# Optimization experiments

Measured on AMD Instinct MI355X. Metric: run time of the kernel, lower is better.

Reference implementation:

```python
import jax, jax.numpy as jnp
import numpy as np
from jax import lax

D_MODEL = 60
D_INNER = 120   # expand=2
D_STATE = 16
D_CONV = 4
DT_RANK = 4     # ceil(60/16)
DEPTH = 2
BATCH = 2
H_IMG = 128
W_IMG = 128
L_SEQ = H_IMG * W_IMG


def setup_inputs() -> dict:
    key = jax.random.key(0)
    ks = jax.random.split(key, 12)
    s = 0.02
    x = jax.random.normal(ks[0], (BATCH, L_SEQ, D_MODEL), jnp.float32)
    ln_w = jnp.ones((DEPTH, D_MODEL), jnp.float32)
    ln_b = jnp.zeros((DEPTH, D_MODEL), jnp.float32)
    in_proj_w = jax.random.normal(ks[1], (DEPTH, 2 * D_INNER, D_MODEL), jnp.float32) * s
    conv_w = jax.random.normal(ks[2], (DEPTH, D_INNER, D_CONV), jnp.float32) * s
    conv_b = jnp.zeros((DEPTH, D_INNER), jnp.float32)
    x_proj_w = jax.random.normal(ks[3], (DEPTH, DT_RANK + 2 * D_STATE, D_INNER), jnp.float32) * s
    dt_proj_w = jax.random.normal(ks[4], (DEPTH, D_INNER, DT_RANK), jnp.float32) * s
    dt_proj_b = jnp.full((DEPTH, D_INNER), -4.0, jnp.float32)  # softplus^-1 of small dt
    A_log = jnp.broadcast_to(
        jnp.log(jnp.arange(1, D_STATE + 1, dtype=jnp.float32))[None, None, :],
        (DEPTH, D_INNER, D_STATE)).copy()
    D_skip = jnp.ones((DEPTH, D_INNER), jnp.float32)
    out_proj_w = jax.random.normal(ks[5], (DEPTH, D_MODEL, D_INNER), jnp.float32) * s
    conv2d_w = jax.random.normal(ks[6], (D_MODEL, D_MODEL, 3, 3), jnp.float32) * s
    conv2d_b = jnp.zeros((D_MODEL,), jnp.float32)
    return {"x": x, "ln_w": ln_w, "ln_b": ln_b, "in_proj_w": in_proj_w,
            "conv_w": conv_w, "conv_b": conv_b, "x_proj_w": x_proj_w,
            "dt_proj_w": dt_proj_w, "dt_proj_b": dt_proj_b, "A_log": A_log,
            "D": D_skip, "out_proj_w": out_proj_w,
            "conv2d_w": conv2d_w, "conv2d_b": conv2d_b,
            "H": H_IMG, "W": W_IMG}


def _layernorm(x, w, b, eps=1e-5):
    mu = jnp.mean(x, axis=-1, keepdims=True)
    var = jnp.mean(jnp.square(x - mu), axis=-1, keepdims=True)
    return (x - mu) * lax.rsqrt(var + eps) * w + b


def _selective_scan(dA, dBx, C):
    # dA, dBx: [B, L, D_INNER, D_STATE]; C: [B, L, D_STATE]
    def step(h, inp):
        dA_t, dBx_t, c_t = inp
        h = dA_t * h + dBx_t                       # [B, D_INNER, D_STATE]
        y = jnp.einsum('bdn,bn->bd', h, c_t)
        return h, y
    h0 = jnp.zeros(dA.shape[:1] + dA.shape[2:], dA.dtype)
    _, ys = lax.scan(step, h0,
                     (dA.transpose(1, 0, 2, 3), dBx.transpose(1, 0, 2, 3),
                      C.transpose(1, 0, 2)))
    return ys.transpose(1, 0, 2)                    # [B, L, D_INNER]


def _mamba(x, in_w, cw, cb, xp_w, dtw, dtb, A_log, D_skip, out_w):
    # x: [B, L, D_MODEL]
    xz = jnp.einsum('bld,ed->ble', x, in_w)         # [B, L, 2*D_INNER]
    xin, z = jnp.split(xz, 2, axis=-1)
    # causal depthwise conv1d over L
    xc = xin.transpose(0, 2, 1)                     # [B, D_INNER, L]
    xc = jnp.pad(xc, ((0, 0), (0, 0), (D_CONV - 1, 0)))
    xc = lax.conv_general_dilated(xc, cw[:, None, :], (1,), 'VALID',
                                  dimension_numbers=('NCH', 'OIH', 'NCH'),
                                  feature_group_count=D_INNER)
    xc = jax.nn.silu(xc + cb[None, :, None]).transpose(0, 2, 1)  # [B, L, D_INNER]
    xdb = jnp.einsum('bld,ed->ble', xc, xp_w)       # [B, L, DT_RANK + 2*D_STATE]
    dt = xdb[..., :DT_RANK]
    Bm = xdb[..., DT_RANK:DT_RANK + D_STATE]
    Cm = xdb[..., DT_RANK + D_STATE:]
    delta = jax.nn.softplus(jnp.einsum('blr,dr->bld', dt, dtw) + dtb)  # [B, L, D_INNER]
    A = -jnp.exp(A_log)                              # [D_INNER, D_STATE]
    dA = jnp.exp(delta[..., None] * A[None, None])   # [B, L, D_INNER, D_STATE]
    dBx = delta[..., None] * Bm[:, :, None, :] * xc[..., None]
    y = _selective_scan(dA, dBx, Cm) + D_skip * xc
    y = y * jax.nn.silu(z)
    return jnp.einsum('ble,de->bld', y, out_w)       # [B, L, D_MODEL]


def reference(x, ln_w, ln_b, in_proj_w, conv_w, conv_b, x_proj_w,
              dt_proj_w, dt_proj_b, A_log, D, out_proj_w,
              conv2d_w, conv2d_b, H, W):
    h = x
    for i in range(DEPTH):
        hn = _layernorm(h, ln_w[i], ln_b[i])
        h = _mamba(hn, in_proj_w[i], conv_w[i], conv_b[i], x_proj_w[i],
                   dt_proj_w[i], dt_proj_b[i], A_log[i], D[i], out_proj_w[i])
    # patch_unembed -> 3x3 conv -> patch_embed, residual add (RMMB)
    b = h.shape[0]
    img = h.transpose(0, 2, 1).reshape(b, D_MODEL, H, W)
    img = lax.conv_general_dilated(img, conv2d_w, (1, 1), 'SAME',
                                   dimension_numbers=('NCHW', 'OIHW', 'NCHW'))
    img = img + conv2d_b[None, :, None, None]
    h = img.reshape(b, D_MODEL, H * W).transpose(0, 2, 1)
    return h + x
```

## Files before the change

### kernel.cpp

```cpp
#include <hip/hip_runtime.h>
#include <math.h>

#define BATCH 2
#define LSEQ 16384
#define DM 60
#define DI 120
#define NCH 512
#define TCH 32
#define HH 128
#define WW 128

typedef __attribute__((ext_vector_type(8))) short bhalf8;
typedef __attribute__((ext_vector_type(4))) short short4v;
typedef __attribute__((ext_vector_type(4))) float f32x4;

__device__ __forceinline__ float sigmoidf_(float x){ return __builtin_amdgcn_rcpf(1.0f + __expf(-x)); }
__device__ __forceinline__ float siluf_(float x){ return x * sigmoidf_(x); }
__device__ __forceinline__ float softplusf_(float x){ return (x > 20.0f) ? x : __logf(1.0f + __expf(x)); }
__device__ __forceinline__ short f2b(float f){
  union{float f; unsigned u;} v; v.f = f;
  unsigned r = (v.u + 0x7fffu + ((v.u >> 16) & 1u)) >> 16;
  return (short)r;
}
__device__ __forceinline__ float b2f(short s){
  union{float f; unsigned u;} v; v.u = ((unsigned)(unsigned short)s) << 16; return v.f;
}

__device__ __forceinline__ void powers8(float r, float* p){
  p[0] = r;
  #pragma unroll
  for (int n = 1; n < 8; n++) p[n] = p[(n-1)>>1] * p[n>>1];
}

__global__ __launch_bounds__(256) void k_pack(
    const float* __restrict__ ipw, const float* __restrict__ xpw,
    const float* __restrict__ opw,
    const float* __restrict__ lnw, const float* __restrict__ lnb,
    short* __restrict__ pk, float* __restrict__ c01)
{
  int i = blockIdx.x*256 + threadIdx.x;
  if (i < 2*240*64){
    int l = i / (240*64);
    int rem = i % (240*64);
    int n = rem / 64, k = rem % 64;
    float v = (k < 60) ? ipw[(size_t)l*14400 + n*60 + k] * lnw[l*60 + k] : 0.f;
    pk[i] = f2b(v);
  } else if (i < 30720 + 2*48*128){
    int j = i - 30720;
    int l = j / (48*128);
    int rem = j % (48*128);
    int n = rem / 128, k = rem % 128;
    float v = (n < 36 && k < 120) ? xpw[(size_t)l*36*120 + n*120 + k] : 0.f;
    pk[i] = f2b(v);
  } else if (i < 43008 + 480){
    int j = i - 43008;
    int l = j / 240, n = j % 240;
    float c1 = 0.f, c0 = 0.f;
    for (int k = 0; k < 60; k++){
      float w = ipw[(size_t)l*14400 + n*60 + k];
      c1 += lnw[l*60+k] * w;
      c0 += lnb[l*60+k] * w;
    }
    c01[(l*240 + n)*2 + 0] = c1;
    c01[(l*240 + n)*2 + 1] = c0;
  } else if (i < 43488 + 2*64*128){
    int j = i - 43488;
    int l = j / 8192;
    int rem = j % 8192;
    int n = rem / 128, k = rem % 128;
    float v = (n < 60 && k < 120) ? opw[(size_t)l*7200 + n*120 + k] : 0.f;
    pk[43008 + j] = f2b(v);
  }
}

__global__ __launch_bounds__(512) void k_lnxp(
    const float* __restrict__ srcf, const short* __restrict__ srcb,
    const short* __restrict__ ipB,
    const float* __restrict__ c01,
    const float* __restrict__ cw, const float* __restrict__ cb,
    const short* __restrict__ xpB,
    const float* __restrict__ dtw, const float* __restrict__ dtb,
    const float* __restrict__ A_log,
    short* __restrict__ zs, short* __restrict__ xcg,
    short* __restrict__ delta, short* __restrict__ BCg,
    float* __restrict__ ap, float* __restrict__ he)
{
  __shared__ __align__(16) char smem[49216];
  short* XB   = (short*)smem;
  short* xcB  = (short*)smem;
  short* xinB = (short*)(smem + 8704);
  float* delLf= (float*)(smem + 8704);
  float* xcf  = (float*)(smem + 24064);
  float* BLf  = (float*)(smem + 39424);
  short* BCL  = (short*)(smem + 41472);
  float* stats= (float*)(smem + 43520);
  float* dtsh = (float*)(smem + 43904);
  float* cwL  = (float*)(smem + 44416);
  float* Wd5T = (float*)(smem + 46336);
  float* cbL  = (float*)(smem + 48256);
  float* bdL  = (float*)(smem + 48736);
  const int tid = threadIdx.x;
  const int wave = tid >> 6, lane = tid & 63;
  const int m = lane & 15, quad = lane >> 4;
  const int row0 = blockIdx.x * 32;
  const int seq0 = (row0 / LSEQ) * LSEQ;
  if (tid < 480){ cwL[tid] = cw[tid]; Wd5T[(tid & 3)*120 + (tid >> 2)] = dtw[tid]; }
  if (tid < 120){ cbL[tid] = cb[tid]; bdL[tid] = dtb[tid]; }
  for (int i = tid; i < 48*16; i += 512){
    int r = i >> 4, g = i & 15;
    int grow = row0 - 3 + r;
    short4v o = {0,0,0,0};
    if (g < 15 && r < 35 && grow >= seq0){
      if (srcb){
        o = *(const short4v*)&srcb[(size_t)grow*60 + g*4];
      } else {
        float4 f = *(const float4*)&srcf[(size_t)grow*60 + g*4];
        o.x = f2b(f.x); o.y = f2b(f.y); o.z = f2b(f.z); o.w = f2b(f.w);
      }
    }
    *(short4v*)&XB[r*72 + g*4] = o;
  }
  __syncthreads();
  {
    const int sub = lane >> 4;
    const int li  = lane & 15;
    #pragma unroll
    for (int it = 0; it < 2; it++){
      int r = it*32 + wave*4 + sub;
      if (r < 48){
        short4v x4 = *(const short4v*)&XB[r*72 + li*4];
        float f0 = b2f(x4.x), f1 = b2f(x4.y), f2 = b2f(x4.z), f3 = b2f(x4.w);
        float sx = (f0 + f1) + (f2 + f3);
        float sq = (f0*f0 + f1*f1) + (f2*f2 + f3*f3);
        #pragma unroll
        for (int off = 1; off < 16; off <<= 1){
          sx += __shfl_xor(sx, off);
          sq += __shfl_xor(sq, off);
        }
        if (li == 0){
          float mu = sx * (1.0f/60.0f);
          float var = fmaxf(sq * (1.0f/60.0f) - mu*mu, 0.f);
          stats[r*2 + 0] = mu;
          stats[r*2 + 1] = rsqrtf(var + 1e-5f);
        }
      }
    }
  }
  __syncthreads();
  for (int t = wave; t < 45; t += 8){
    int mtile = t / 15, ntile = t % 15;
    f32x4 acc = {0.f,0.f,0.f,0.f};
    #pragma unroll
    for (int ks = 0; ks < 2; ks++){
      bhalf8 a = *(const bhalf8*)&XB[(mtile*16 + m)*72 + ks*32 + quad*8];
      bhalf8 b = *(const bhalf8*)&ipB[(ntile*16 + m)*64 + ks*32 + quad*8];
      acc = __builtin_amdgcn_mfma_f32_16x16x32_bf16(a, b, acc, 0, 0, 0);
    }
    int n = ntile*16 + m;
    float2 cc = *(const float2*)&c01[n*2];
    float c1v = cc.x, c0v = cc.y;
    #pragma unroll
    for (int reg = 0; reg < 4; reg++){
      int r = mtile*16 + quad*4 + reg;
      int grow = row0 - 3 + r;
      bool valid = (r < 35) && (grow >= seq0);
      float mu = stats[r*2], rs = stats[r*2+1];
      float val = rs*(acc[reg] - mu*c1v) + c0v;
      if (!valid) val = 0.f;
      if (n < 120){
        xinB[r*136 + n] = f2b(val);
      } else if (r >= 3 && r < 35){
        zs[(size_t)(row0 - 3 + r)*120 + (n - 120)] = f2b(siluf_(val));
      }
    }
  }
  __syncthreads();
  for (int i = tid; i < 960; i += 512){
    int r = i/30, c4 = (i%30)*4;
    float4 cbv = *(const float4*)&cbL[c4];
    float4 w0 = *(const float4*)&cwL[(c4+0)*4];
    float4 w1 = *(const float4*)&cwL[(c4+1)*4];
    float4 w2 = *(const float4*)&cwL[(c4+2)*4];
    float4 w3 = *(const float4*)&cwL[(c4+3)*4];
    short4v x0 = *(const short4v*)&xinB[(r+0)*136 + c4];
    short4v x1 = *(const short4v*)&xinB[(r+1)*136 + c4];
    short4v x2 = *(const short4v*)&xinB[(r+2)*136 + c4];
    short4v x3 = *(const short4v*)&xinB[(r+3)*136 + c4];
    float a0 = cbv.x + w0.x*b2f(x0.x) + w0.y*b2f(x1.x) + w0.z*b2f(x2.x) + w0.w*b2f(x3.x);
    float a1 = cbv.y + w1.x*b2f(x0.y) + w1.y*b2f(x1.y) + w1.z*b2f(x2.y) + w1.w*b2f(x3.y);
    float a2 = cbv.z + w2.x*b2f(x0.z) + w2.y*b2f(x1.z) + w2.z*b2f(x2.z) + w2.w*b2f(x3.z);
    float a3 = cbv.w + w3.x*b2f(x0.w) + w3.y*b2f(x1.w) + w3.z*b2f(x2.w) + w3.w*b2f(x3.w);
    a0 = siluf_(a0); a1 = siluf_(a1); a2 = siluf_(a2); a3 = siluf_(a3);
    float4 fo; fo.x = a0; fo.y = a1; fo.z = a2; fo.w = a3;
    *(float4*)&xcf[r*120 + c4] = fo;
    short4v o;
    o.x = f2b(a0); o.y = f2b(a1); o.z = f2b(a2); o.w = f2b(a3);
    *(short4v*)&xcB[r*136 + c4] = o;
  }
  for (int i = tid; i < 32*8; i += 512)
    xcB[(i >> 3)*136 + 120 + (i & 7)] = 0;
  __syncthreads();
  for (int t = wave; t < 6; t += 8){
    int mtile = t / 3, ntile = t % 3;
    f32x4 acc = {0.f,0.f,0.f,0.f};
    #pragma unroll
    for (int ks = 0; ks < 4; ks++){
      bhalf8 a = *(const bhalf8*)&xcB[(mtile*16 + m)*136 + ks*32 + quad*8];
      bhalf8 b = *(const bhalf8*)&xpB[(ntile*16 + m)*128 + ks*32 + quad*8];
      acc = __builtin_amdgcn_mfma_f32_16x16x32_bf16(a, b, acc, 0, 0, 0);
    }
    int n = ntile*16 + m;
    #pragma unroll
    for (int reg = 0; reg < 4; reg++){
      int r = mtile*16 + quad*4 + reg;
      float val = acc[reg];
      if (n < 4)        dtsh[r*4 + n] = val;
      else if (n < 36){
        BCL[r*32 + (n - 4)] = f2b(val);
        if (n < 20) BLf[r*16 + (n - 4)] = val;
      }
    }
  }
  __syncthreads();
  for (int i = tid; i < 960; i += 512){
    int row = i/30, c4 = (i%30)*4;
    float4 t4 = *(const float4*)&dtsh[row*4];
    float4 w0 = *(const float4*)&Wd5T[0*120 + c4];
    float4 w1 = *(const float4*)&Wd5T[1*120 + c4];
    float4 w2 = *(const float4*)&Wd5T[2*120 + c4];
    float4 w3 = *(const float4*)&Wd5T[3*120 + c4];
    float4 bb = *(const float4*)&bdL[c4];
    float4 dd;
    dd.x = softplusf_(bb.x + t4.x*w0.x + t4.y*w1.x + t4.z*w2.x + t4.w*w3.x);
    dd.y = softplusf_(bb.y + t4.x*w0.y + t4.y*w1.y + t4.z*w2.y + t4.w*w3.y);
    dd.z = softplusf_(bb.z + t4.x*w0.z + t4.y*w1.z + t4.z*w2.z + t4.w*w3.z);
    dd.w = softplusf_(bb.w + t4.x*w0.w + t4.y*w1.w + t4.z*w2.w + t4.w*w3.w);
    *(float4*)&delLf[row*120 + c4] = dd;
    short4v o;
    o.x = f2b(dd.x); o.y = f2b(dd.y); o.z = f2b(dd.z); o.w = f2b(dd.w);
    *(short4v*)&delta[(size_t)(row0 + row)*120 + c4] = o;
  }
  __syncthreads();
  for (int i = tid; i < 960; i += 512){
    int r = i/30, off = (i%30)*4;
    *(short4v*)&xcg[(size_t)(row0 + r)*120 + off] = *(const short4v*)&xcB[r*136 + off];
  }
  for (int i = tid; i < 256; i += 512)
    *(short4v*)&BCg[(size_t)row0*32 + i*4] = *(const short4v*)&BCL[i*4];
  if (tid < 480){
    const int d = tid >> 2, q = tid & 3, n0 = q << 2;
    const int b = row0 / LSEQ;
    const int cglob = (row0 % LSEQ) >> 5;
    float A2[4], h[4];
    const float A20 = -__expf(A_log[d*16]) * 1.44269504f;
    #pragma unroll
    for (int n = 0; n < 4; n++){
      A2[n] = -__expf(A_log[d*16 + n0 + n]) * 1.44269504f;
      h[n] = 0.f;
    }
    bool fastp = true;
    #pragma unroll
    for (int n = 0; n < 4; n++)
      fastp = fastp && (fabsf(A2[n] - (n0+n+1)*A20) <= 1e-4f*fabsf(A2[n]));
    int fp = fastp ? 1 : 0;
    fp &= __shfl_xor(fp, 1);
    fp &= __shfl_xor(fp, 2);
    const int sh1 = q & 1, sh2 = q & 2;
    int base = (cglob*BATCH + b)*(DI*16) + d*16 + n0;
    if (fp){
      float P = 1.f;
      for (int t = 0; t < 32; t += 2){
        float d1 = delLf[t*120 + d],     d2 = delLf[(t+1)*120 + d];
        float x1 = xcf[t*120 + d],       x2 = xcf[(t+1)*120 + d];
        float dx1 = d1*x1, dx2 = d2*x2;
        float r2s = exp2f(d2*A20);
        float rr  = exp2f((d1+d2)*A20);
        P *= rr;
        float c1 = rr*rr, c2 = c1*rr, c3 = c1*c1;
        float sc = sh1 ? c3 : 1.0f; if (sh2) sc *= c3*c3;
        float p1 = r2s*r2s, p2 = p1*r2s, p3 = p1*p1;
        float s2 = sh1 ? p3 : 1.0f; if (sh2) s2 *= p3*p3;
        float4 b1 = *(const float4*)&BLf[t*16 + n0];
        float4 b2 = *(const float4*)&BLf[(t+1)*16 + n0];
        float ad0 = (s2*r2s)*dx1*b1.x + dx2*b2.x;
        float ad1 = (s2*p1 )*dx1*b1.y + dx2*b2.y;
        float ad2 = (s2*p2 )*dx1*b1.z + dx2*b2.z;
        float ad3 = (s2*p3 )*dx1*b1.w + dx2*b2.w;
        h[0] = (sc*rr)*h[0] + ad0;
        h[1] = (sc*c1)*h[1] + ad1;
        h[2] = (sc*c2)*h[2] + ad2;
        h[3] = (sc*c3)*h[3] + ad3;
      }
      float P1 = P*P;
      float P2 = P1*P, P3 = P1*P1;
      float sP = sh1 ? P3 : 1.0f;
      if (sh2) sP *= P3*P3;
      float apv[4] = {sP*P, sP*P1, sP*P2, sP*P3};
      *(float4*)&ap[base] = *(float4*)&apv[0];
      *(float4*)&he[base] = *(float4*)&h[0];
    } else {
      float apv[4] = {1.f,1.f,1.f,1.f};
      for (int t = 0; t < 32; t++){
        float del = delLf[t*120 + d];
        float dx = del * xcf[t*120 + d];
        #pragma unroll
        for (int n = 0; n < 4; n++){
          float dA = exp2f(del * A2[n]);
          apv[n] *= dA;
          h[n] = dA*h[n] + dx*BLf[t*16 + n0 + n];
        }
      }
      *(float4*)&ap[base] = *(float4*)&apv[0];
      *(float4*)&he[base] = *(float4*)&h[0];
    }
  }
}

__global__ __launch_bounds__(256) void k_scan2(float* __restrict__ ap, const float* __restrict__ he)
{
  __shared__ float aggA[16*17];
  __shared__ float aggB[16*17];
  const int tid = threadIdx.x;
  const int n = tid & 15, j = tid >> 4;
  const int sbase = blockIdx.x*16 + n;
  const int stride = BATCH*DI*16;
  {
    float A = 1.f, B = 0.f;
    int idx = (j*32)*stride + sbase;
    #pragma unroll 4
    for (int k = 0; k < 32; k++){
      float a = ap[idx], h = he[idx];
      B = a*B + h;
      A *= a;
      idx += stride;
    }
    aggA[n*17 + j] = A;
    aggB[n*17 + j] = B;
  }
  __syncthreads();
  if (tid < 16){
    float B = 0.f;
    #pragma unroll
    for (int jj = 0; jj < 16; jj++){
      float Af = aggA[tid*17 + jj];
      float Bf = aggB[tid*17 + jj];
      aggB[tid*17 + jj] = B;
      B = Af*B + Bf;
    }
  }
  __syncthreads();
  {
    float H = aggB[n*17 + j];
    int idx = (j*32)*stride + sbase;
    #pragma unroll 4
    for (int k = 0; k < 32; k++){
      float a = ap[idx], h = he[idx];
      ap[idx] = H;
      H = a*H + h;
      idx += stride;
    }
  }
}

__global__ __launch_bounds__(256) void k_scan3o(
    const short* __restrict__ delta, const short* __restrict__ xc,
    const short* __restrict__ BCg, const short* __restrict__ zs,
    const float* __restrict__ h0, const float* __restrict__ A_log,
    const float* __restrict__ Dsk, const short* __restrict__ opB,
    short* __restrict__ hout)
{
  __shared__ float BCl[TCH*32];
  __shared__ __align__(16) short yL[TCH*136];
  __shared__ __align__(16) short dL[TCH*120];
  __shared__ __align__(16) short xL[TCH*120];
  __shared__ __align__(16) short zL[TCH*120];
  const int tid = threadIdx.x;
  const int wave = tid >> 6, lane = tid & 63;
  const int m = lane & 15, quad = lane >> 4;
  const int c = blockIdx.x % NCH, b = blockIdx.x / NCH;
  const size_t rowbase = (size_t)b*LSEQ + (size_t)c*TCH;
  for (int i = tid; i < 960; i += 256)
    *(short4v*)&dL[i*4] = *(const short4v*)&delta[rowbase*DI + i*4];
  for (int i = tid; i < 960; i += 256)
    *(short4v*)&xL[i*4] = *(const short4v*)&xc[rowbase*DI + i*4];
  for (int i = tid; i < 960; i += 256)
    *(short4v*)&zL[i*4] = *(const short4v*)&zs[rowbase*DI + i*4];
  for (int i = tid; i < TCH*8; i += 256){
    short4v v = *(const short4v*)&BCg[rowbase*32 + i*4];
    float4 f; f.x = b2f(v.x); f.y = b2f(v.y); f.z = b2f(v.z); f.w = b2f(v.w);
    *(float4*)&BCl[i*4] = f;
  }
  for (int i = tid; i < TCH*4; i += 256){
    short4v z = {0,0,0,0};
    *(short4v*)&yL[(i >> 2)*136 + 120 + (i & 3)*4] = z;
  }
  __syncthreads();
  if (tid < 240){
    const int d = tid >> 1, half = tid & 1, n0 = half << 3;
    float A2[8], h[8];
    const int base = (c*BATCH + b)*(DI*16) + d*16 + n0;
    const float A20 = -__expf(A_log[d*16]) * 1.44269504f;
    #pragma unroll
    for (int n = 0; n < 8; n++){
      A2[n] = -__expf(A_log[d*16 + n0 + n]) * 1.44269504f;
      h[n] = h0[base + n];
    }
    bool fastp = true;
    #pragma unroll
    for (int n = 0; n < 8; n++)
      fastp = fastp && (fabsf(A2[n] - (n0+n+1)*A20) <= 1e-4f*fabsf(A2[n]));
    int fp = fastp ? 1 : 0;
    fp &= __shfl_xor(fp, 1);
    const float Dv = Dsk[d];
    if (fp){
      for (int t = 0; t < TCH; t++){
        float del = b2f(dL[t*120 + d]);
        float xcv = b2f(xL[t*120 + d]);
        float zv  = b2f(zL[t*120 + d]);
        float dx = del * xcv;
        float r = exp2f(del * A20);
        float p8[8]; powers8(r, p8);
        float s = half ? p8[7] : 1.0f;
        float4 b0 = *(const float4*)&BCl[t*32 + n0];
        float4 b1 = *(const float4*)&BCl[t*32 + n0 + 4];
        h[0] = (s*p8[0])*h[0] + dx*b0.x;  h[1] = (s*p8[1])*h[1] + dx*b0.y;
        h[2] = (s*p8[2])*h[2] + dx*b0.z;  h[3] = (s*p8[3])*h[3] + dx*b0.w;
        h[4] = (s*p8[4])*h[4] + dx*b1.x;  h[5] = (s*p8[5])*h[5] + dx*b1.y;
        h[6] = (s*p8[6])*h[6] + dx*b1.z;  h[7] = (s*p8[7])*h[7] + dx*b1.w;
        float4 c0 = *(const float4*)&BCl[t*32 + 16 + n0];
        float4 c1 = *(const float4*)&BCl[t*32 + 20 + n0];
        float acc = h[0]*c0.x + h[1]*c0.y + h[2]*c0.z + h[3]*c0.w
                  + h[4]*c1.x + h[5]*c1.y + h[6]*c1.z + h[7]*c1.w;
        acc += __shfl_xor(acc, 1);
        if (!half) yL[t*136 + d] = f2b((acc + Dv*xcv) * zv);
      }
    } else {
      for (int t = 0; t < TCH; t++){
        float del = b2f(dL[t*120 + d]);
        float xcv = b2f(xL[t*120 + d]);
        float zv  = b2f(zL[t*120 + d]);
        float dx = del * xcv;
        float acc = 0.f;
        #pragma unroll
        for (int n = 0; n < 8; n++){
          float dA = exp2f(del * A2[n]);
          h[n] = dA*h[n] + dx*BCl[t*32 + n0 + n];
          acc += h[n]*BCl[t*32 + 16 + n0 + n];
        }
        acc += __shfl_xor(acc, 1);
        if (!half) yL[t*136 + d] = f2b((acc + Dv*xcv) * zv);
      }
    }
  }
  __syncthreads();
  for (int t = wave; t < 8; t += 4){
    const int mtile = t >> 2, ntile = t & 3;
    f32x4 acc = {0.f,0.f,0.f,0.f};
    #pragma unroll
    for (int ks = 0; ks < 4; ks++){
      bhalf8 a  = *(const bhalf8*)&yL[(mtile*16 + m)*136 + ks*32 + quad*8];
      bhalf8 bb = *(const bhalf8*)&opB[(ntile*16 + m)*128 + ks*32 + quad*8];
      acc = __builtin_amdgcn_mfma_f32_16x16x32_bf16(a, bb, acc, 0, 0, 0);
    }
    const int n = ntile*16 + m;
    if (n < 60){
      #pragma unroll
      for (int reg = 0; reg < 4; reg++){
        int r = mtile*16 + quad*4 + reg;
        hout[(rowbase + r)*60 + n] = f2b(acc[reg]);
      }
    }
  }
}

__global__ __launch_bounds__(256) void k_wB(const float* __restrict__ w, short* __restrict__ wB)
{
  int i = blockIdx.x*256 + threadIdx.x;
  if (i >= 9*64*64) return;
  int ci = i & 63, co = (i >> 6) & 63, tap = i >> 12;
  float v = 0.f;
  if (co < 60 && ci < 60) v = w[((size_t)co*60 + ci)*9 + tap];
  wB[i] = f2b(v);
}

__global__ __launch_bounds__(256) void k_conv2d(
    const short* __restrict__ hin, const short* __restrict__ wB,
    const float* __restrict__ cb, const float* __restrict__ xres,
    float* __restrict__ out)
{
  __shared__ short tile[3*66*72];
  const int tid = threadIdx.x;
  const int blk = blockIdx.x;
  const int xhalf = blk & 1;
  const int yy = (blk >> 1) & 127;
  const int b = blk >> 8;
  const int x0 = xhalf*64;
  for (int i = tid; i < 3*66*18; i += 256){
    int g = i % 18;
    int xx = (i / 18) % 66;
    int row = i / (18*66);
    int gy = yy - 1 + row, gx = x0 - 1 + xx;
    short4v v = {0,0,0,0};
    if (g < 15 && gy >= 0 && gy < HH && gx >= 0 && gx < WW)
      v = *(const short4v*)&hin[((size_t)b*LSEQ + gy*WW + gx)*60 + g*4];
    *(short4v*)&tile[(row*66 + xx)*72 + g*4] = v;
  }
  __syncthreads();
  const int wave = tid >> 6, lane = tid & 63;
  const int m = lane & 15, quad = lane >> 4;
  f32x4 acc0 = {0.f,0.f,0.f,0.f}, acc1 = {0.f,0.f,0.f,0.f};
  f32x4 acc2 = {0.f,0.f,0.f,0.f}, acc3 = {0.f,0.f,0.f,0.f};
  #pragma unroll
  for (int tap = 0; tap < 9; tap++){
    const int ky = tap/3, kx = tap%3;
    const short* arow = &tile[(ky*66 + wave*16 + m + kx)*72];
    const short* brow = wB + tap*4096;
    #pragma unroll
    for (int kh = 0; kh < 2; kh++){
      const int k0 = kh*32 + quad*8;
      bhalf8 a = *(const bhalf8*)(arow + k0);
      bhalf8 b0 = *(const bhalf8*)(brow + (0*16 + m)*64 + k0);
      bhalf8 b1 = *(const bhalf8*)(brow + (1*16 + m)*64 + k0);
      bhalf8 b2 = *(const bhalf8*)(brow + (2*16 + m)*64 + k0);
      bhalf8 b3 = *(const bhalf8*)(brow + (3*16 + m)*64 + k0);
      acc0 = __builtin_amdgcn_mfma_f32_16x16x32_bf16(a, b0, acc0, 0, 0, 0);
      acc1 = __builtin_amdgcn_mfma_f32_16x16x32_bf16(a, b1, acc1, 0, 0, 0);
      acc2 = __builtin_amdgcn_mfma_f32_16x16x32_bf16(a, b2, acc2, 0, 0, 0);
      acc3 = __builtin_amdgcn_mfma_f32_16x16x32_bf16(a, b3, acc3, 0, 0, 0);
    }
  }
  const size_t rowb = (size_t)b*LSEQ + yy*WW + x0;
  f32x4 accs[4] = {acc0, acc1, acc2, acc3};
  #pragma unroll
  for (int nt = 0; nt < 4; nt++){
    int co = nt*16 + m;
    if (co < 60){
      float bias = cb[co];
      #pragma unroll
      for (int reg = 0; reg < 4; reg++){
        int px = wave*16 + quad*4 + reg;
        size_t o = (rowb + px)*60 + co;
        out[o] = accs[nt][reg] + bias + xres[o];
      }
    }
  }
}

extern "C" void kernel_launch(void* const* d_in, const int* in_sizes, int n_in,
                              void* d_out, int out_size, void* d_ws, size_t ws_size,
                              hipStream_t stream)
{
  const float* x      = (const float*)d_in[0];
  const float* ln_w   = (const float*)d_in[1];
  const float* ln_b   = (const float*)d_in[2];
  const float* ipw    = (const float*)d_in[3];
  const float* cw     = (const float*)d_in[4];
  const float* cb1    = (const float*)d_in[5];
  const float* xpw    = (const float*)d_in[6];
  const float* dtw    = (const float*)d_in[7];
  const float* dtb    = (const float*)d_in[8];
  const float* A_log  = (const float*)d_in[9];
  const float* Dsk    = (const float*)d_in[10];
  const float* opw    = (const float*)d_in[11];
  const float* c2w    = (const float*)d_in[12];
  const float* c2b    = (const float*)d_in[13];
  float* out = (float*)d_out;

  char* ws = (char*)d_ws;
  size_t off = 0;
  short* zsb   = (short*)(ws + off); off += (size_t)BATCH*LSEQ*DI*2;
  short* xcb   = (short*)(ws + off); off += (size_t)BATCH*LSEQ*DI*2;
  short* dlt   = (short*)(ws + off); off += (size_t)BATCH*LSEQ*DI*2;
  short* BCg   = (short*)(ws + off); off += (size_t)BATCH*LSEQ*32*2;
  float* apb   = (float*)(ws + off); off += (size_t)NCH*BATCH*DI*16*4;
  float* heb   = (float*)(ws + off); off += (size_t)NCH*BATCH*DI*16*4;
  short* hcur  = (short*)(ws + off); off += (size_t)BATCH*LSEQ*DM*2;
  short* wBb   = (short*)(ws + off); off += (size_t)9*64*64*2;
  short* pkb   = (short*)(ws + off); off += (size_t)(2*240*64 + 2*48*128 + 2*64*128)*2;
  float* c01b  = (float*)(ws + off); off += (size_t)2*240*2*4;

  const int rows = BATCH*LSEQ;
  k_pack<<<(43008 + 480 + 16384 + 255)/256, 256, 0, stream>>>(ipw, xpw, opw, ln_w, ln_b, pkb, c01b);
  for (int layer = 0; layer < 2; layer++){
    const float* srcf = (layer == 0) ? x : nullptr;
    const short* srcb = (layer == 0) ? nullptr : hcur;
    k_lnxp<<<rows/32, 512, 0, stream>>>(srcf, srcb,
                                        pkb + (size_t)layer*240*64,
                                        c01b + (size_t)layer*240*2,
                                        cw + layer*DI*4, cb1 + layer*DI,
                                        pkb + 30720 + (size_t)layer*48*128,
                                        dtw + (size_t)layer*DI*4, dtb + layer*DI,
                                        A_log + (size_t)layer*DI*16,
                                        zsb, xcb, dlt, BCg, apb, heb);
    k_scan2<<<BATCH*DI, 256, 0, stream>>>(apb, heb);
    k_scan3o<<<BATCH*NCH, 256, 0, stream>>>(dlt, xcb, BCg, zsb, apb, A_log + (size_t)layer*DI*16,
                                            Dsk + layer*DI, pkb + 43008 + (size_t)layer*8192, hcur);
  }
  k_wB<<<(9*64*64+255)/256, 256, 0, stream>>>(c2w, wBb);
  k_conv2d<<<BATCH*HH*2, 256, 0, stream>>>(hcur, wBb, c2b, x, out);
}
```

Measured before the change: 257.8 us.

## Split chunk-local scan out of k_lnxp into separate k_scanP kernel

The chunk-local selective-scan pass (per-chunk decay products and end states) moves out of the fused LN/projection kernel into a new kernel. That kernel reloads delta, xc and B as bf16 from global memory. This cuts k_lnxp shared memory from about 49KB to 29.5KB and drops its fp32 staging buffers, which should raise occupancy. The cost is an extra launch and extra global traffic, and the scan now reads bf16-rounded delta and x instead of fp32, which slightly changes numerics.

```diff
diff --git a/kernel.cpp b/kernel.cpp
--- a/kernel.cpp
+++ b/kernel.cpp
@@ -80,25 +80,20 @@
     const float* __restrict__ cw, const float* __restrict__ cb,
     const short* __restrict__ xpB,
     const float* __restrict__ dtw, const float* __restrict__ dtb,
-    const float* __restrict__ A_log,
     short* __restrict__ zs, short* __restrict__ xcg,
-    short* __restrict__ delta, short* __restrict__ BCg,
-    float* __restrict__ ap, float* __restrict__ he)
-{
-  __shared__ __align__(16) char smem[49216];
+    short* __restrict__ delta, short* __restrict__ BCg)
+{
+  __shared__ __align__(16) char smem[29504];
   short* XB   = (short*)smem;
   short* xcB  = (short*)smem;
   short* xinB = (short*)(smem + 8704);
-  float* delLf= (float*)(smem + 8704);
-  float* xcf  = (float*)(smem + 24064);
-  float* BLf  = (float*)(smem + 39424);
-  short* BCL  = (short*)(smem + 41472);
-  float* stats= (float*)(smem + 43520);
-  float* dtsh = (float*)(smem + 43904);
-  float* cwL  = (float*)(smem + 44416);
-  float* Wd5T = (float*)(smem + 46336);
-  float* cbL  = (float*)(smem + 48256);
-  float* bdL  = (float*)(smem + 48736);
+  short* BCL  = (short*)(smem + 21760);
+  float* stats= (float*)(smem + 23808);
+  float* dtsh = (float*)(smem + 24192);
+  float* cwL  = (float*)(smem + 24704);
+  float* Wd5T = (float*)(smem + 26624);
+  float* cbL  = (float*)(smem + 28544);
+  float* bdL  = (float*)(smem + 29024);
   const int tid = threadIdx.x;
   const int wave = tid >> 6, lane = tid & 63;
   const int m = lane & 15, quad = lane >> 4;
@@ -190,11 +185,8 @@
     float a1 = cbv.y + w1.x*b2f(x0.y) + w1.y*b2f(x1.y) + w1.z*b2f(x2.y) + w1.w*b2f(x3.y);
     float a2 = cbv.z + w2.x*b2f(x0.z) + w2.y*b2f(x1.z) + w2.z*b2f(x2.z) + w2.w*b2f(x3.z);
     float a3 = cbv.w + w3.x*b2f(x0.w) + w3.y*b2f(x1.w) + w3.z*b2f(x2.w) + w3.w*b2f(x3.w);
-    a0 = siluf_(a0); a1 = siluf_(a1); a2 = siluf_(a2); a3 = siluf_(a3);
-    float4 fo; fo.x = a0; fo.y = a1; fo.z = a2; fo.w = a3;
-    *(float4*)&xcf[r*120 + c4] = fo;
     short4v o;
-    o.x = f2b(a0); o.y = f2b(a1); o.z = f2b(a2); o.w = f2b(a3);
+    o.x = f2b(siluf_(a0)); o.y = f2b(siluf_(a1)); o.z = f2b(siluf_(a2)); o.w = f2b(siluf_(a3));
     *(short4v*)&xcB[r*136 + c4] = o;
   }
   for (int i = tid; i < 32*8; i += 512)
@@ -215,10 +207,7 @@
       int r = mtile*16 + quad*4 + reg;
       float val = acc[reg];
       if (n < 4)        dtsh[r*4 + n] = val;
-      else if (n < 36){
-        BCL[r*32 + (n - 4)] = f2b(val);
-        if (n < 20) BLf[r*16 + (n - 4)] = val;
-      }
+      else if (n < 36)  BCL[r*32 + (n - 4)] = f2b(val);
     }
   }
   __syncthreads();
@@ -230,25 +219,44 @@
     float4 w2 = *(const float4*)&Wd5T[2*120 + c4];
     float4 w3 = *(const float4*)&Wd5T[3*120 + c4];
     float4 bb = *(const float4*)&bdL[c4];
-    float4 dd;
-    dd.x = softplusf_(bb.x + t4.x*w0.x + t4.y*w1.x + t4.z*w2.x + t4.w*w3.x);
-    dd.y = softplusf_(bb.y + t4.x*w0.y + t4.y*w1.y + t4.z*w2.y + t4.w*w3.y);
-    dd.z = softplusf_(bb.z + t4.x*w0.z + t4.y*w1.z + t4.z*w2.z + t4.w*w3.z);
-    dd.w = softplusf_(bb.w + t4.x*w0.w + t4.y*w1.w + t4.z*w2.w + t4.w*w3.w);
-    *(float4*)&delLf[row*120 + c4] = dd;
     short4v o;
-    o.x = f2b(dd.x); o.y = f2b(dd.y); o.z = f2b(dd.z); o.w = f2b(dd.w);
+    o.x = f2b(softplusf_(bb.x + t4.x*w0.x + t4.y*w1.x + t4.z*w2.x + t4.w*w3.x));
+    o.y = f2b(softplusf_(bb.y + t4.x*w0.y + t4.y*w1.y + t4.z*w2.y + t4.w*w3.y));
+    o.z = f2b(softplusf_(bb.z + t4.x*w0.z + t4.y*w1.z + t4.z*w2.z + t4.w*w3.z));
+    o.w = f2b(softplusf_(bb.w + t4.x*w0.w + t4.y*w1.w + t4.z*w2.w + t4.w*w3.w));
     *(short4v*)&delta[(size_t)(row0 + row)*120 + c4] = o;
   }
-  __syncthreads();
   for (int i = tid; i < 960; i += 512){
     int r = i/30, off = (i%30)*4;
     *(short4v*)&xcg[(size_t)(row0 + r)*120 + off] = *(const short4v*)&xcB[r*136 + off];
   }
   for (int i = tid; i < 256; i += 512)
     *(short4v*)&BCg[(size_t)row0*32 + i*4] = *(const short4v*)&BCL[i*4];
+}
+
+__global__ __launch_bounds__(512) void k_scanP(
+    const short* __restrict__ delta, const short* __restrict__ xc,
+    const short* __restrict__ BCg, const float* __restrict__ A_log,
+    float* __restrict__ ap, float* __restrict__ he)
+{
+  __shared__ __align__(16) short dL[32*120];
+  __shared__ __align__(16) short xL[32*120];
+  __shared__ __align__(16) float BLf[32*16];
+  const int tid = threadIdx.x;
+  const int row0 = blockIdx.x * 32;
+  for (int i = tid; i < 960; i += 512)
+    *(short4v*)&dL[i*4] = *(const short4v*)&delta[(size_t)row0*120 + i*4];
+  for (int i = tid; i < 960; i += 512)
+    *(short4v*)&xL[i*4] = *(const short4v*)&xc[(size_t)row0*120 + i*4];
+  for (int i = tid; i < 128; i += 512){
+    int r = i >> 2, g = i & 3;
+    short4v v = *(const short4v*)&BCg[(size_t)(row0 + r)*32 + g*4];
+    float4 f; f.x = b2f(v.x); f.y = b2f(v.y); f.z = b2f(v.z); f.w = b2f(v.w);
+    *(float4*)&BLf[r*16 + g*4] = f;
+  }
+  __syncthreads();
   if (tid < 480){
-    const int d = tid >> 2, q = tid & 3, n0 = q << 2;
+    const int q = tid / 120, d = tid - q*120, n0 = q << 2;
     const int b = row0 / LSEQ;
     const int cglob = (row0 % LSEQ) >> 5;
     float A2[4], h[4];
@@ -262,16 +270,13 @@
     #pragma unroll
     for (int n = 0; n < 4; n++)
       fastp = fastp && (fabsf(A2[n] - (n0+n+1)*A20) <= 1e-4f*fabsf(A2[n]));
-    int fp = fastp ? 1 : 0;
-    fp &= __shfl_xor(fp, 1);
-    fp &= __shfl_xor(fp, 2);
     const int sh1 = q & 1, sh2 = q & 2;
     int base = (cglob*BATCH + b)*(DI*16) + d*16 + n0;
-    if (fp){
+    if (fastp){
       float P = 1.f;
       for (int t = 0; t < 32; t += 2){
-        float d1 = delLf[t*120 + d],     d2 = delLf[(t+1)*120 + d];
-        float x1 = xcf[t*120 + d],       x2 = xcf[(t+1)*120 + d];
+        float d1 = b2f(dL[t*120 + d]),     d2 = b2f(dL[(t+1)*120 + d]);
+        float x1 = b2f(xL[t*120 + d]),     x2 = b2f(xL[(t+1)*120 + d]);
         float dx1 = d1*x1, dx2 = d2*x2;
         float r2s = exp2f(d2*A20);
         float rr  = exp2f((d1+d2)*A20);
@@ -301,8 +306,8 @@
     } else {
       float apv[4] = {1.f,1.f,1.f,1.f};
       for (int t = 0; t < 32; t++){
-        float del = delLf[t*120 + d];
-        float dx = del * xcf[t*120 + d];
+        float del = b2f(dL[t*120 + d]);
+        float dx = del * b2f(xL[t*120 + d]);
         #pragma unroll
         for (int n = 0; n < 4; n++){
           float dA = exp2f(del * A2[n]);
@@ -590,8 +595,8 @@
                                         cw + layer*DI*4, cb1 + layer*DI,
                                         pkb + 30720 + (size_t)layer*48*128,
                                         dtw + (size_t)layer*DI*4, dtb + layer*DI,
-                                        A_log + (size_t)layer*DI*16,
-                                        zsb, xcb, dlt, BCg, apb, heb);
+                                        zsb, xcb, dlt, BCg);
+    k_scanP<<<rows/32, 512, 0, stream>>>(dlt, xcb, BCg, A_log + (size_t)layer*DI*16, apb, heb);
     k_scan2<<<BATCH*DI, 256, 0, stream>>>(apb, heb);
     k_scan3o<<<BATCH*NCH, 256, 0, stream>>>(dlt, xcb, BCg, zsb, apb, A_log + (size_t)layer*DI*16,
                                             Dsk + layer*DI, pkb + 43008 + (size_t)layer*8192, hcur);
```

Measured after the change: 265.3 us. 1.03x slower.
